# Kernel tuning notes

Measured on AMD Instinct MI355X. Metric: run time of the kernel, lower is better.

## Reference

```python
import jax, jax.numpy as jnp
import numpy as np

EPS = 1e-12  # matches F.normalize eps

def _l2norm(x):
    n = jnp.sqrt(jnp.sum(x * x, axis=-1, keepdims=True))
    return x / jnp.maximum(n, EPS)

def setup_inputs() -> dict:
    key = jax.random.key(0)
    k1, k2, k3, k4 = jax.random.split(key, 4)
    Bq, Lq, H = 32, 32, 768
    ppq = 8
    Bd, Ld = Bq * ppq, 512
    dim = 128
    q_hidden = jax.random.normal(k1, (Bq, Lq, H), dtype=jnp.float32)
    d_hidden = jax.random.normal(k2, (Bd, Ld, H), dtype=jnp.float32)
    W = jax.random.normal(k3, (dim, H), dtype=jnp.float32) * (1.0 / np.sqrt(H))
    d_mask = jax.random.randint(k4, (Bd, Ld), 0, 2).astype(bool)
    d_mask = d_mask.at[:, 0].set(True)  # guarantee >=1 valid token per doc
    return {"q_hidden": q_hidden, "d_hidden": d_hidden, "W": W,
            "d_mask": d_mask, "ppq": ppq}

def reference(q_hidden, d_hidden, W, d_mask, ppq):
    # linear projection (no bias) + L2 normalize, as in query()/doc()
    q = _l2norm(jnp.einsum('bqh,dh->bqd', q_hidden, W))        # [Bq, Lq, dim]
    d = _l2norm(jnp.einsum('bkh,dh->bkd', d_hidden, W))        # [Bd, Ld, dim]
    d = d * d_mask[..., None].astype(d.dtype)                  # zero masked tokens
    qd = jnp.repeat(q, ppq, axis=0)                            # [Bd, Lq, dim]
    sim = jnp.einsum('bqd,bkd->bqk', qd, d)                    # cosine MaxSim scores
    sim = jnp.where(d_mask[:, None, :], sim, -jnp.inf)         # mask doc tokens
    return jnp.sum(jnp.max(sim, axis=-1), axis=-1)             # [Bd]
```

## Files before the change

kernel.cpp:

```cpp
#include <hip/hip_runtime.h>
#include <math.h>

#define H    768
#define NT   24
#define DIM  128
#define LQ   32
#define LD   512
#define BM   128
#define EPSF 1e-12f

typedef _Float16 f16x8 __attribute__((ext_vector_type(8)));
typedef _Float16 f16x4 __attribute__((ext_vector_type(4)));
typedef float    f32x4 __attribute__((ext_vector_type(4)));

static __device__ __forceinline__ unsigned short h2u(_Float16 h) {
    return __builtin_bit_cast(unsigned short, h);
}

#define GLOAD_LDS16(g, l) __builtin_amdgcn_global_load_lds(                    \
    (const __attribute__((address_space(1))) unsigned int*)(const void*)(g),   \
    (__attribute__((address_space(3))) unsigned int*)(void*)(l), 16, 0, 0)

__global__ __launch_bounds__(256) void wconv_kernel(
    const float* __restrict__ W, unsigned short* __restrict__ wsW,
    float* __restrict__ WT)
{
    const int ks  = blockIdx.x;
    const int tid = threadIdx.x;
    #pragma unroll 4
    for (int i = 0; i < 16; ++i) {
        const int idx = tid + i * 256;
        const int row = idx >> 5, col = idx & 31;
        const float x = W[(size_t)row * H + ks * 32 + col];
        const int colS = (((col >> 3) ^ ((row >> 1) & 3)) << 3) | (col & 7);
        wsW[((size_t)ks * 128 + row) * 32 + colS] = h2u((_Float16)x);
        WT[((size_t)ks * 32 + col) * DIM + row] = x;
    }
}

__global__ __launch_bounds__(128) void qproj_kernel(
    const float* __restrict__ qh, const float* __restrict__ WT,
    unsigned short* __restrict__ qn)
{
    const int blk = blockIdx.x;
    const int tid = threadIdx.x;
    __shared__ float rows[4][H];
    __shared__ float red[128];

    const float4* src = (const float4*)(qh + (size_t)blk * 4 * H);
    float4*       dst = (float4*)&rows[0][0];
    for (int i = tid; i < 4 * H / 4; i += 128) dst[i] = src[i];
    __syncthreads();

    float acc[4] = {0.f, 0.f, 0.f, 0.f};
    #pragma unroll 8
    for (int h = 0; h < H; ++h) {
        const float wv = WT[(size_t)h * DIM + tid];
        acc[0] += wv * rows[0][h];
        acc[1] += wv * rows[1][h];
        acc[2] += wv * rows[2][h];
        acc[3] += wv * rows[3][h];
    }
    #pragma unroll
    for (int j = 0; j < 4; ++j) {
        red[tid] = acc[j] * acc[j];
        __syncthreads();
        for (int s = 64; s > 0; s >>= 1) {
            if (tid < s) red[tid] += red[tid + s];
            __syncthreads();
        }
        const float inv = 1.0f / fmaxf(sqrtf(red[0]), EPSF);
        qn[((size_t)blk * 4 + j) * DIM + tid] = h2u((_Float16)(acc[j] * inv));
        __syncthreads();
    }
}

struct Smem {
    union {
        struct {
            unsigned short A[2][BM][32];
            unsigned short Wt[2][128][32];
        } g;
        unsigned short C[BM][DIM];
    } u;
    float         pnorm[2][BM];
    unsigned char mk[BM];
    float         pmax[LQ][4];
};

__global__ __launch_bounds__(256, 4) void docgemm_kernel(
    const float* __restrict__ dh, const unsigned short* __restrict__ wsW,
    const int* __restrict__ dmask, const unsigned short* __restrict__ qn,
    float* __restrict__ part, const int* __restrict__ ppq_p)
{
    __shared__ Smem sm;
    const int blk = blockIdx.x;
    const int b   = blk >> 2;
    const int c   = blk & 3;
    const int tid = threadIdx.x;
    const int w   = tid >> 6;
    const int wm  = w >> 1, wn = w & 1;
    const int l   = tid & 63;
    const int g   = l >> 4;
    const int r15 = l & 15;
    const int ppq = ppq_p[0];

    const int r0   = tid >> 3;
    const int seg0 = tid & 7;
    const int aswz = (r0 >> 1) & 3;
    const int coli = (((seg0 >> 1) ^ aswz) << 3) | ((seg0 & 1) << 2);

    const float* Abase = dh + ((size_t)b * LD + (size_t)c * BM) * H;

    f32x4 acc[4][4];
    #pragma unroll
    for (int m = 0; m < 4; ++m)
        #pragma unroll
        for (int n = 0; n < 4; ++n)
            acc[m][n] = (f32x4){0.f, 0.f, 0.f, 0.f};

    float4 avA[4];

    {
        const char* wt   = (const char*)wsW;
        char*       wdst = (char*)&sm.u.g.Wt[0][0][0];
        GLOAD_LDS16(wt + tid * 16,        wdst + w * 1024);
        GLOAD_LDS16(wt + 4096 + tid * 16, wdst + 4096 + w * 1024);
        __builtin_amdgcn_sched_barrier(0);
        #pragma unroll
        for (int i = 0; i < 4; ++i)
            avA[i] = *(const float4*)(Abase + (size_t)(r0 + i * 32) * H + seg0 * 4);
        #pragma unroll
        for (int i = 0; i < 4; ++i) {
            const int row = r0 + i * 32;
            f16x4 h;
            h[0] = (_Float16)avA[i].x; h[1] = (_Float16)avA[i].y;
            h[2] = (_Float16)avA[i].z; h[3] = (_Float16)avA[i].w;
            *(f16x4*)&sm.u.g.A[0][row][coli] = h;
        }
        #pragma unroll
        for (int i = 0; i < 4; ++i)
            avA[i] = *(const float4*)(Abase + (size_t)(r0 + i * 32) * H + 32 + seg0 * 4);
        asm volatile("s_waitcnt vmcnt(4) lgkmcnt(0)" ::: "memory");
        __builtin_amdgcn_sched_barrier(0);
        __builtin_amdgcn_s_barrier();
        __builtin_amdgcn_sched_barrier(0);
    }

    for (int t = 0; t < NT; ++t) {
        const int cur = t & 1, nxt = cur ^ 1;

        if (t + 1 < NT) {
            const char* wt   = (const char*)wsW + (size_t)(t + 1) * 8192;
            char*       wdst = (char*)&sm.u.g.Wt[nxt][0][0];
            GLOAD_LDS16(wt + tid * 16,        wdst + w * 1024);
            GLOAD_LDS16(wt + 4096 + tid * 16, wdst + 4096 + w * 1024);
        }
        __builtin_amdgcn_sched_barrier(0);

        f16x8 ah[4];
        #pragma unroll
        for (int m = 0; m < 4; ++m) {
            const int row = wm * 64 + m * 16 + r15;
            const int sl  = (g ^ ((row >> 1) & 3)) * 8;
            ah[m] = *(const f16x8*)&sm.u.g.A[cur][row][sl];
        }
        __builtin_amdgcn_s_setprio(1);
        #pragma unroll
        for (int n = 0; n < 4; ++n) {
            const int row = wn * 64 + n * 16 + r15;
            const int sl  = (g ^ ((row >> 1) & 3)) * 8;
            f16x8 bh = *(const f16x8*)&sm.u.g.Wt[cur][row][sl];
            #pragma unroll
            for (int m = 0; m < 4; ++m)
                acc[m][n] = __builtin_amdgcn_mfma_f32_16x16x32_f16(ah[m], bh, acc[m][n], 0, 0, 0);
        }
        __builtin_amdgcn_s_setprio(0);

        if (t + 1 < NT) {
            #pragma unroll
            for (int i = 0; i < 4; ++i) {
                const int row = r0 + i * 32;
                f16x4 h;
                h[0] = (_Float16)avA[i].x; h[1] = (_Float16)avA[i].y;
                h[2] = (_Float16)avA[i].z; h[3] = (_Float16)avA[i].w;
                *(f16x4*)&sm.u.g.A[nxt][row][coli] = h;
            }
        }
        if (t + 2 < NT) {
            const int k0n = (t + 2) * 32;
            #pragma unroll
            for (int i = 0; i < 4; ++i)
                avA[i] = *(const float4*)(Abase + (size_t)(r0 + i * 32) * H + k0n + seg0 * 4);
        }

        if (t + 2 < NT) {
            asm volatile("s_waitcnt vmcnt(4) lgkmcnt(0)" ::: "memory");
        } else {
            asm volatile("s_waitcnt vmcnt(0) lgkmcnt(0)" ::: "memory");
        }
        __builtin_amdgcn_sched_barrier(0);
        __builtin_amdgcn_s_barrier();
        __builtin_amdgcn_sched_barrier(0);
    }

    #pragma unroll
    for (int m = 0; m < 4; ++m) {
        const int tokb = wm * 64 + m * 16 + g * 4;
        #pragma unroll
        for (int n = 0; n < 4; ++n) {
            const int dim = wn * 64 + n * 16 + r15;
            #pragma unroll
            for (int r = 0; r < 4; ++r) {
                const int tok  = tokb + r;
                const int slot = (dim >> 3) ^ (tok & 7);
                sm.u.C[tok][slot * 8 + (dim & 7)] = h2u((_Float16)acc[m][n][r]);
            }
        }
    }
    #pragma unroll
    for (int m = 0; m < 4; ++m) {
        #pragma unroll
        for (int r = 0; r < 4; ++r) {
            float s = 0.f;
            #pragma unroll
            for (int n = 0; n < 4; ++n) s += acc[m][n][r] * acc[m][n][r];
            s += __shfl_xor(s, 1); s += __shfl_xor(s, 2);
            s += __shfl_xor(s, 4); s += __shfl_xor(s, 8);
            if (r15 == 0) sm.pnorm[wn][wm * 64 + m * 16 + g * 4 + r] = s;
        }
    }
    if (tid < BM) sm.mk[tid] = (unsigned char)(dmask[(size_t)b * LD + c * BM + tid] != 0);
    __syncthreads();

    const unsigned short* qb = qn + (size_t)(b / ppq) * LQ * DIM;
    const int t0 = w * 32 + r15, t1 = t0 + 16;
    const float inv0 = 1.0f / fmaxf(sqrtf(sm.pnorm[0][t0] + sm.pnorm[1][t0]), EPSF);
    const float inv1 = 1.0f / fmaxf(sqrtf(sm.pnorm[0][t1] + sm.pnorm[1][t1]), EPSF);

    f32x4 sacc[2][2];
    #pragma unroll
    for (int m = 0; m < 2; ++m)
        #pragma unroll
        for (int n = 0; n < 2; ++n)
            sacc[m][n] = (f32x4){0.f, 0.f, 0.f, 0.f};
    #pragma unroll
    for (int ks = 0; ks < 4; ++ks) {
        f16x8 qa[2], cb[2];
        #pragma unroll
        for (int m = 0; m < 2; ++m)
            qa[m] = *(const f16x8*)(qb + (size_t)(m * 16 + r15) * DIM + ks * 32 + g * 8);
        #pragma unroll
        for (int n = 0; n < 2; ++n) {
            const int row  = w * 32 + n * 16 + r15;
            const int slot = (ks * 4 + g) ^ (row & 7);
            cb[n] = *(const f16x8*)&sm.u.C[row][slot * 8];
        }
        #pragma unroll
        for (int m = 0; m < 2; ++m)
            #pragma unroll
            for (int n = 0; n < 2; ++n)
                sacc[m][n] = __builtin_amdgcn_mfma_f32_16x16x32_f16(qa[m], cb[n], sacc[m][n], 0, 0, 0);
    }

    const int m0 = sm.mk[t0], m1 = sm.mk[t1];
    #pragma unroll
    for (int m = 0; m < 2; ++m) {
        #pragma unroll
        for (int r = 0; r < 4; ++r) {
            float v0 = m0 ? sacc[m][0][r] * inv0 : -INFINITY;
            float v1 = m1 ? sacc[m][1][r] * inv1 : -INFINITY;
            float vmax = fmaxf(v0, v1);
            vmax = fmaxf(vmax, __shfl_xor(vmax, 1));
            vmax = fmaxf(vmax, __shfl_xor(vmax, 2));
            vmax = fmaxf(vmax, __shfl_xor(vmax, 4));
            vmax = fmaxf(vmax, __shfl_xor(vmax, 8));
            if (r15 == 0) sm.pmax[m * 16 + g * 4 + r][w] = vmax;
        }
    }
    __syncthreads();
    if (tid < LQ) {
        float mv = fmaxf(fmaxf(sm.pmax[tid][0], sm.pmax[tid][1]),
                         fmaxf(sm.pmax[tid][2], sm.pmax[tid][3]));
        part[(size_t)blk * 32 + tid] = mv;
    }
}

__global__ __launch_bounds__(64) void final_kernel(
    const float* __restrict__ part, float* __restrict__ out)
{
    const int b = blockIdx.x;
    const int q = threadIdx.x & 31;
    const float* p = part + (size_t)b * 128;
    float m = fmaxf(fmaxf(p[q], p[32 + q]), fmaxf(p[64 + q], p[96 + q]));
    #pragma unroll
    for (int off = 1; off < 32; off <<= 1) m += __shfl_xor(m, off);
    if (threadIdx.x == 0) out[b] = m;
}

extern "C" void kernel_launch(void* const* d_in, const int* in_sizes, int n_in,
                              void* d_out, int out_size, void* d_ws, size_t ws_size,
                              hipStream_t stream) {
    const float* qh    = (const float*)d_in[0];
    const float* dh    = (const float*)d_in[1];
    const float* W     = (const float*)d_in[2];
    const int*   dmask = (const int*)d_in[3];
    const int*   ppq   = (const int*)d_in[4];
    float*       out   = (float*)d_out;

    unsigned short* wsW  = (unsigned short*)d_ws;
    float*          WT   = (float*)((char*)d_ws + 196608);
    unsigned short* qn   = (unsigned short*)((char*)d_ws + 589824);
    float*          part = (float*)((char*)d_ws + 851968);

    const int nq = in_sizes[0] / H;
    const int Bd = out_size;

    wconv_kernel<<<NT, 256, 0, stream>>>(W, wsW, WT);
    qproj_kernel<<<nq / 4, 128, 0, stream>>>(qh, WT, qn);
    docgemm_kernel<<<Bd * 4, 256, 0, stream>>>(dh, wsW, dmask, qn, part, ppq);
    final_kernel<<<Bd, 64, 0, stream>>>(part, out);
}
```

Baseline: 131.5 us.

## Double K-tile to 64, use 8-wave doc GEMM blocks, split qproj reduction

The doc projection GEMM now uses a K step of 64 instead of 32, so there are 12 pipeline iterations instead of 24. It runs 512-thread blocks arranged as a 2x4 wave grid, with a matching XOR swizzle for the wider LDS rows. The MaxSim epilogue is remapped so each of the 8 waves handles 16 tokens, and the query projection splits the H reduction across two thread halves. The aim is fewer barriers per byte streamed and more memory-level parallelism on the bandwidth-bound fp32 doc read. The cost is double the LDS per block, which limits residency to 2 blocks per CU and may reduce latency hiding.

```diff
diff --git a/kernel.cpp b/kernel.cpp
--- a/kernel.cpp
+++ b/kernel.cpp
@@ -2,7 +2,7 @@
 #include <math.h>
 
 #define H    768
-#define NT   24
+#define NT   12
 #define DIM  128
 #define LQ   32
 #define LD   512
@@ -27,50 +27,59 @@
 {
     const int ks  = blockIdx.x;
     const int tid = threadIdx.x;
-    #pragma unroll 4
-    for (int i = 0; i < 16; ++i) {
+    #pragma unroll 8
+    for (int i = 0; i < 32; ++i) {
         const int idx = tid + i * 256;
-        const int row = idx >> 5, col = idx & 31;
-        const float x = W[(size_t)row * H + ks * 32 + col];
-        const int colS = (((col >> 3) ^ ((row >> 1) & 3)) << 3) | (col & 7);
-        wsW[((size_t)ks * 128 + row) * 32 + colS] = h2u((_Float16)x);
-        WT[((size_t)ks * 32 + col) * DIM + row] = x;
-    }
-}
-
-__global__ __launch_bounds__(128) void qproj_kernel(
+        const int row = idx >> 6, col = idx & 63;
+        const float x = W[(size_t)row * H + ks * 64 + col];
+        const int colS = (((col >> 3) ^ (row & 7)) << 3) | (col & 7);
+        wsW[((size_t)ks * 128 + row) * 64 + colS] = h2u((_Float16)x);
+        WT[((size_t)ks * 64 + col) * DIM + row] = x;
+    }
+}
+
+__global__ __launch_bounds__(256) void qproj_kernel(
     const float* __restrict__ qh, const float* __restrict__ WT,
     unsigned short* __restrict__ qn)
 {
     const int blk = blockIdx.x;
     const int tid = threadIdx.x;
+    const int td  = tid & 127;
+    const int hp  = tid >> 7;
     __shared__ float rows[4][H];
+    __shared__ float psum[2][4][128];
     __shared__ float red[128];
 
     const float4* src = (const float4*)(qh + (size_t)blk * 4 * H);
     float4*       dst = (float4*)&rows[0][0];
-    for (int i = tid; i < 4 * H / 4; i += 128) dst[i] = src[i];
+    for (int i = tid; i < 4 * H / 4; i += 256) dst[i] = src[i];
     __syncthreads();
 
     float acc[4] = {0.f, 0.f, 0.f, 0.f};
+    const int h0 = hp * (H / 2);
     #pragma unroll 8
-    for (int h = 0; h < H; ++h) {
-        const float wv = WT[(size_t)h * DIM + tid];
+    for (int h = h0; h < h0 + H / 2; ++h) {
+        const float wv = WT[(size_t)h * DIM + td];
         acc[0] += wv * rows[0][h];
         acc[1] += wv * rows[1][h];
         acc[2] += wv * rows[2][h];
         acc[3] += wv * rows[3][h];
     }
     #pragma unroll
+    for (int j = 0; j < 4; ++j) psum[hp][j][td] = acc[j];
+    __syncthreads();
+
+    #pragma unroll
     for (int j = 0; j < 4; ++j) {
-        red[tid] = acc[j] * acc[j];
+        const float val = psum[0][j][td] + psum[1][j][td];
+        if (hp == 0) red[td] = val * val;
         __syncthreads();
         for (int s = 64; s > 0; s >>= 1) {
             if (tid < s) red[tid] += red[tid + s];
             __syncthreads();
         }
         const float inv = 1.0f / fmaxf(sqrtf(red[0]), EPSF);
-        qn[((size_t)blk * 4 + j) * DIM + tid] = h2u((_Float16)(acc[j] * inv));
+        if (hp == 0) qn[((size_t)blk * 4 + j) * DIM + td] = h2u((_Float16)(val * inv));
         __syncthreads();
     }
 }
@@ -78,17 +87,17 @@
 struct Smem {
     union {
         struct {
-            unsigned short A[2][BM][32];
-            unsigned short Wt[2][128][32];
+            unsigned short A[2][BM][64];
+            unsigned short Wt[2][128][64];
         } g;
         unsigned short C[BM][DIM];
     } u;
-    float         pnorm[2][BM];
+    float         pnorm[4][BM];
     unsigned char mk[BM];
-    float         pmax[LQ][4];
+    float         pmax[LQ][8];
 };
 
-__global__ __launch_bounds__(256, 4) void docgemm_kernel(
+__global__ __launch_bounds__(512, 2) void docgemm_kernel(
     const float* __restrict__ dh, const unsigned short* __restrict__ wsW,
     const int* __restrict__ dmask, const unsigned short* __restrict__ qn,
     float* __restrict__ part, const int* __restrict__ ppq_p)
@@ -99,24 +108,25 @@
     const int c   = blk & 3;
     const int tid = threadIdx.x;
     const int w   = tid >> 6;
-    const int wm  = w >> 1, wn = w & 1;
+    const int wm  = w >> 2;
+    const int wn  = w & 3;
     const int l   = tid & 63;
     const int g   = l >> 4;
     const int r15 = l & 15;
     const int ppq = ppq_p[0];
 
-    const int r0   = tid >> 3;
-    const int seg0 = tid & 7;
-    const int aswz = (r0 >> 1) & 3;
-    const int coli = (((seg0 >> 1) ^ aswz) << 3) | ((seg0 & 1) << 2);
+    const int r0   = tid >> 4;
+    const int seg0 = tid & 15;
+    const int wgr  = seg0 >> 1;
+    const int wsub = (seg0 & 1) * 8;
 
     const float* Abase = dh + ((size_t)b * LD + (size_t)c * BM) * H;
 
-    f32x4 acc[4][4];
+    f32x4 acc[4][2];
     #pragma unroll
     for (int m = 0; m < 4; ++m)
         #pragma unroll
-        for (int n = 0; n < 4; ++n)
+        for (int n = 0; n < 2; ++n)
             acc[m][n] = (f32x4){0.f, 0.f, 0.f, 0.f};
 
     float4 avA[4];
@@ -125,7 +135,7 @@
         const char* wt   = (const char*)wsW;
         char*       wdst = (char*)&sm.u.g.Wt[0][0][0];
         GLOAD_LDS16(wt + tid * 16,        wdst + w * 1024);
-        GLOAD_LDS16(wt + 4096 + tid * 16, wdst + 4096 + w * 1024);
+        GLOAD_LDS16(wt + 8192 + tid * 16, wdst + 8192 + w * 1024);
         __builtin_amdgcn_sched_barrier(0);
         #pragma unroll
         for (int i = 0; i < 4; ++i)
@@ -136,11 +146,11 @@
             f16x4 h;
             h[0] = (_Float16)avA[i].x; h[1] = (_Float16)avA[i].y;
             h[2] = (_Float16)avA[i].z; h[3] = (_Float16)avA[i].w;
-            *(f16x4*)&sm.u.g.A[0][row][coli] = h;
+            *(f16x4*)((char*)&sm.u.g.A[0][0][0] + row * 128 + (((wgr ^ (row & 7)) << 4) | wsub)) = h;
         }
         #pragma unroll
         for (int i = 0; i < 4; ++i)
-            avA[i] = *(const float4*)(Abase + (size_t)(r0 + i * 32) * H + 32 + seg0 * 4);
+            avA[i] = *(const float4*)(Abase + (size_t)(r0 + i * 32) * H + 64 + seg0 * 4);
         asm volatile("s_waitcnt vmcnt(4) lgkmcnt(0)" ::: "memory");
         __builtin_amdgcn_sched_barrier(0);
         __builtin_amdgcn_s_barrier();
@@ -151,29 +161,34 @@
         const int cur = t & 1, nxt = cur ^ 1;
 
         if (t + 1 < NT) {
-            const char* wt   = (const char*)wsW + (size_t)(t + 1) * 8192;
+            const char* wt   = (const char*)wsW + (size_t)(t + 1) * 16384;
             char*       wdst = (char*)&sm.u.g.Wt[nxt][0][0];
             GLOAD_LDS16(wt + tid * 16,        wdst + w * 1024);
-            GLOAD_LDS16(wt + 4096 + tid * 16, wdst + 4096 + w * 1024);
-        }
-        __builtin_amdgcn_sched_barrier(0);
-
-        f16x8 ah[4];
-        #pragma unroll
-        for (int m = 0; m < 4; ++m) {
-            const int row = wm * 64 + m * 16 + r15;
-            const int sl  = (g ^ ((row >> 1) & 3)) * 8;
-            ah[m] = *(const f16x8*)&sm.u.g.A[cur][row][sl];
-        }
+            GLOAD_LDS16(wt + 8192 + tid * 16, wdst + 8192 + w * 1024);
+        }
+        __builtin_amdgcn_sched_barrier(0);
+
+        const char* Ab = (const char*)&sm.u.g.A[cur][0][0];
+        const char* Wb = (const char*)&sm.u.g.Wt[cur][0][0];
+        f16x8 ah[2][4];
+        #pragma unroll
+        for (int ksub = 0; ksub < 2; ++ksub)
+            #pragma unroll
+            for (int m = 0; m < 4; ++m) {
+                const int row = wm * 64 + m * 16 + r15;
+                ah[ksub][m] = *(const f16x8*)(Ab + row * 128 + ((((ksub * 4 + g)) ^ (row & 7)) << 4));
+            }
         __builtin_amdgcn_s_setprio(1);
         #pragma unroll
-        for (int n = 0; n < 4; ++n) {
-            const int row = wn * 64 + n * 16 + r15;
-            const int sl  = (g ^ ((row >> 1) & 3)) * 8;
-            f16x8 bh = *(const f16x8*)&sm.u.g.Wt[cur][row][sl];
-            #pragma unroll
-            for (int m = 0; m < 4; ++m)
-                acc[m][n] = __builtin_amdgcn_mfma_f32_16x16x32_f16(ah[m], bh, acc[m][n], 0, 0, 0);
+        for (int ksub = 0; ksub < 2; ++ksub) {
+            #pragma unroll
+            for (int n = 0; n < 2; ++n) {
+                const int row = wn * 32 + n * 16 + r15;
+                f16x8 bh = *(const f16x8*)(Wb + row * 128 + ((((ksub * 4 + g)) ^ (row & 7)) << 4));
+                #pragma unroll
+                for (int m = 0; m < 4; ++m)
+                    acc[m][n] = __builtin_amdgcn_mfma_f32_16x16x32_f16(ah[ksub][m], bh, acc[m][n], 0, 0, 0);
+            }
         }
         __builtin_amdgcn_s_setprio(0);
 
@@ -184,11 +199,11 @@
                 f16x4 h;
                 h[0] = (_Float16)avA[i].x; h[1] = (_Float16)avA[i].y;
                 h[2] = (_Float16)avA[i].z; h[3] = (_Float16)avA[i].w;
-                *(f16x4*)&sm.u.g.A[nxt][row][coli] = h;
+                *(f16x4*)((char*)&sm.u.g.A[nxt][0][0] + row * 128 + (((wgr ^ (row & 7)) << 4) | wsub)) = h;
             }
         }
         if (t + 2 < NT) {
-            const int k0n = (t + 2) * 32;
+            const int k0n = (t + 2) * 64;
             #pragma unroll
             for (int i = 0; i < 4; ++i)
                 avA[i] = *(const float4*)(Abase + (size_t)(r0 + i * 32) * H + k0n + seg0 * 4);
@@ -208,8 +223,8 @@
     for (int m = 0; m < 4; ++m) {
         const int tokb = wm * 64 + m * 16 + g * 4;
         #pragma unroll
-        for (int n = 0; n < 4; ++n) {
-            const int dim = wn * 64 + n * 16 + r15;
+        for (int n = 0; n < 2; ++n) {
+            const int dim = wn * 32 + n * 16 + r15;
             #pragma unroll
             for (int r = 0; r < 4; ++r) {
                 const int tok  = tokb + r;
@@ -222,9 +237,7 @@
     for (int m = 0; m < 4; ++m) {
         #pragma unroll
         for (int r = 0; r < 4; ++r) {
-            float s = 0.f;
-            #pragma unroll
-            for (int n = 0; n < 4; ++n) s += acc[m][n][r] * acc[m][n][r];
+            float s = acc[m][0][r] * acc[m][0][r] + acc[m][1][r] * acc[m][1][r];
             s += __shfl_xor(s, 1); s += __shfl_xor(s, 2);
             s += __shfl_xor(s, 4); s += __shfl_xor(s, 8);
             if (r15 == 0) sm.pnorm[wn][wm * 64 + m * 16 + g * 4 + r] = s;
@@ -234,54 +247,42 @@
     __syncthreads();
 
     const unsigned short* qb = qn + (size_t)(b / ppq) * LQ * DIM;
-    const int t0 = w * 32 + r15, t1 = t0 + 16;
-    const float inv0 = 1.0f / fmaxf(sqrtf(sm.pnorm[0][t0] + sm.pnorm[1][t0]), EPSF);
-    const float inv1 = 1.0f / fmaxf(sqrtf(sm.pnorm[0][t1] + sm.pnorm[1][t1]), EPSF);
-
-    f32x4 sacc[2][2];
-    #pragma unroll
-    for (int m = 0; m < 2; ++m)
-        #pragma unroll
-        for (int n = 0; n < 2; ++n)
-            sacc[m][n] = (f32x4){0.f, 0.f, 0.f, 0.f};
+    const int tok = w * 16 + r15;
+    const float inv = 1.0f / fmaxf(sqrtf(sm.pnorm[0][tok] + sm.pnorm[1][tok] +
+                                         sm.pnorm[2][tok] + sm.pnorm[3][tok]), EPSF);
+    const int msk = sm.mk[tok];
+
+    f32x4 sacc[2];
+    sacc[0] = (f32x4){0.f, 0.f, 0.f, 0.f};
+    sacc[1] = (f32x4){0.f, 0.f, 0.f, 0.f};
     #pragma unroll
     for (int ks = 0; ks < 4; ++ks) {
-        f16x8 qa[2], cb[2];
-        #pragma unroll
-        for (int m = 0; m < 2; ++m)
-            qa[m] = *(const f16x8*)(qb + (size_t)(m * 16 + r15) * DIM + ks * 32 + g * 8);
-        #pragma unroll
-        for (int n = 0; n < 2; ++n) {
-            const int row  = w * 32 + n * 16 + r15;
-            const int slot = (ks * 4 + g) ^ (row & 7);
-            cb[n] = *(const f16x8*)&sm.u.C[row][slot * 8];
-        }
-        #pragma unroll
-        for (int m = 0; m < 2; ++m)
-            #pragma unroll
-            for (int n = 0; n < 2; ++n)
-                sacc[m][n] = __builtin_amdgcn_mfma_f32_16x16x32_f16(qa[m], cb[n], sacc[m][n], 0, 0, 0);
-    }
-
-    const int m0 = sm.mk[t0], m1 = sm.mk[t1];
+        const int slot = (ks * 4 + g) ^ (tok & 7);
+        f16x8 cb = *(const f16x8*)&sm.u.C[tok][slot * 8];
+        #pragma unroll
+        for (int m = 0; m < 2; ++m) {
+            f16x8 qa = *(const f16x8*)(qb + (size_t)(m * 16 + r15) * DIM + ks * 32 + g * 8);
+            sacc[m] = __builtin_amdgcn_mfma_f32_16x16x32_f16(qa, cb, sacc[m], 0, 0, 0);
+        }
+    }
+
     #pragma unroll
     for (int m = 0; m < 2; ++m) {
         #pragma unroll
         for (int r = 0; r < 4; ++r) {
-            float v0 = m0 ? sacc[m][0][r] * inv0 : -INFINITY;
-            float v1 = m1 ? sacc[m][1][r] * inv1 : -INFINITY;
-            float vmax = fmaxf(v0, v1);
-            vmax = fmaxf(vmax, __shfl_xor(vmax, 1));
-            vmax = fmaxf(vmax, __shfl_xor(vmax, 2));
-            vmax = fmaxf(vmax, __shfl_xor(vmax, 4));
-            vmax = fmaxf(vmax, __shfl_xor(vmax, 8));
-            if (r15 == 0) sm.pmax[m * 16 + g * 4 + r][w] = vmax;
+            float v = msk ? sacc[m][r] * inv : -INFINITY;
+            v = fmaxf(v, __shfl_xor(v, 1));
+            v = fmaxf(v, __shfl_xor(v, 2));
+            v = fmaxf(v, __shfl_xor(v, 4));
+            v = fmaxf(v, __shfl_xor(v, 8));
+            if (r15 == 0) sm.pmax[m * 16 + g * 4 + r][w] = v;
         }
     }
     __syncthreads();
     if (tid < LQ) {
-        float mv = fmaxf(fmaxf(sm.pmax[tid][0], sm.pmax[tid][1]),
-                         fmaxf(sm.pmax[tid][2], sm.pmax[tid][3]));
+        float mv = sm.pmax[tid][0];
+        #pragma unroll
+        for (int j = 1; j < 8; ++j) mv = fmaxf(mv, sm.pmax[tid][j]);
         part[(size_t)blk * 32 + tid] = mv;
     }
 }
@@ -317,7 +318,7 @@
     const int Bd = out_size;
 
     wconv_kernel<<<NT, 256, 0, stream>>>(W, wsW, WT);
-    qproj_kernel<<<nq / 4, 128, 0, stream>>>(qh, WT, qn);
-    docgemm_kernel<<<Bd * 4, 256, 0, stream>>>(dh, wsW, dmask, qn, part, ppq);
+    qproj_kernel<<<nq / 4, 256, 0, stream>>>(qh, WT, qn);
+    docgemm_kernel<<<Bd * 4, 512, 0, stream>>>(dh, wsW, dmask, qn, part, ppq);
     final_kernel<<<Bd, 64, 0, stream>>>(part, out);
 }
```

Result: slower. 194.1 us (+47.6%).

## Deepen doc GEMM A-tile register prefetch and split query projection over hidden dimension

Applied to the files above, without the earlier changes.

The doc GEMM main loop is unrolled by two and uses two register buffers for the fp32 A tiles. Global loads now run three K-steps ahead and are issued before the MFMA block, so more HBM latency is hidden on this bandwidth-bound stream. The query projection kernel doubles its threads and splits the 768-wide reduction into two halves combined through shared memory, to shorten its serial dot-product loop. The extra live float4 registers raise VGPR pressure under launch_bounds(256,4), which could cost occupancy or cause spills.

```diff
diff --git a/kernel.cpp b/kernel.cpp
--- a/kernel.cpp
+++ b/kernel.cpp
@@ -38,39 +38,48 @@
     }
 }
 
-__global__ __launch_bounds__(128) void qproj_kernel(
+__global__ __launch_bounds__(256) void qproj_kernel(
     const float* __restrict__ qh, const float* __restrict__ WT,
     unsigned short* __restrict__ qn)
 {
     const int blk = blockIdx.x;
     const int tid = threadIdx.x;
+    const int td  = tid & 127;
+    const int hp  = tid >> 7;
     __shared__ float rows[4][H];
+    __shared__ float psum[2][4][128];
     __shared__ float red[128];
 
     const float4* src = (const float4*)(qh + (size_t)blk * 4 * H);
     float4*       dst = (float4*)&rows[0][0];
-    for (int i = tid; i < 4 * H / 4; i += 128) dst[i] = src[i];
+    for (int i = tid; i < 4 * H / 4; i += 256) dst[i] = src[i];
     __syncthreads();
 
     float acc[4] = {0.f, 0.f, 0.f, 0.f};
+    const int h0 = hp * (H / 2);
     #pragma unroll 8
-    for (int h = 0; h < H; ++h) {
-        const float wv = WT[(size_t)h * DIM + tid];
+    for (int h = h0; h < h0 + H / 2; ++h) {
+        const float wv = WT[(size_t)h * DIM + td];
         acc[0] += wv * rows[0][h];
         acc[1] += wv * rows[1][h];
         acc[2] += wv * rows[2][h];
         acc[3] += wv * rows[3][h];
     }
     #pragma unroll
+    for (int j = 0; j < 4; ++j) psum[hp][j][td] = acc[j];
+    __syncthreads();
+
+    #pragma unroll
     for (int j = 0; j < 4; ++j) {
-        red[tid] = acc[j] * acc[j];
+        const float val = psum[0][j][td] + psum[1][j][td];
+        if (hp == 0) red[td] = val * val;
         __syncthreads();
         for (int s = 64; s > 0; s >>= 1) {
             if (tid < s) red[tid] += red[tid + s];
             __syncthreads();
         }
         const float inv = 1.0f / fmaxf(sqrtf(red[0]), EPSF);
-        qn[((size_t)blk * 4 + j) * DIM + tid] = h2u((_Float16)(acc[j] * inv));
+        if (hp == 0) qn[((size_t)blk * 4 + j) * DIM + td] = h2u((_Float16)(val * inv));
         __syncthreads();
     }
 }
@@ -87,6 +96,62 @@
     unsigned char mk[BM];
     float         pmax[LQ][4];
 };
+
+#define KSTEP(T, CUR, NXT, AV)                                                  \
+  {                                                                             \
+    if ((T) + 1 < NT) {                                                         \
+      const char* wt_   = (const char*)wsW + (size_t)((T) + 1) * 8192;          \
+      char*       wdst_ = (char*)&sm.u.g.Wt[NXT][0][0];                         \
+      GLOAD_LDS16(wt_ + tid * 16,        wdst_ + w * 1024);                     \
+      GLOAD_LDS16(wt_ + 4096 + tid * 16, wdst_ + 4096 + w * 1024);              \
+    }                                                                           \
+    __builtin_amdgcn_sched_barrier(0);                                          \
+    if ((T) + 1 < NT) {                                                         \
+      _Pragma("unroll")                                                         \
+      for (int i = 0; i < 4; ++i) {                                             \
+        const int row_ = r0 + i * 32;                                           \
+        f16x4 h_;                                                               \
+        h_[0] = (_Float16)AV[i].x; h_[1] = (_Float16)AV[i].y;                   \
+        h_[2] = (_Float16)AV[i].z; h_[3] = (_Float16)AV[i].w;                   \
+        *(f16x4*)&sm.u.g.A[NXT][row_][coli] = h_;                               \
+      }                                                                         \
+    }                                                                           \
+    if ((T) + 3 < NT) {                                                         \
+      const int k0n_ = ((T) + 3) * 32;                                          \
+      _Pragma("unroll")                                                         \
+      for (int i = 0; i < 4; ++i)                                               \
+        AV[i] = *(const float4*)(Abase + (size_t)(r0 + i * 32) * H + k0n_ + seg0 * 4); \
+    }                                                                           \
+    __builtin_amdgcn_sched_barrier(0);                                          \
+    {                                                                           \
+      f16x8 ah_[4];                                                             \
+      _Pragma("unroll")                                                         \
+      for (int m = 0; m < 4; ++m) {                                             \
+        const int row_ = wm * 64 + m * 16 + r15;                                \
+        const int sl_  = (g ^ ((row_ >> 1) & 3)) * 8;                           \
+        ah_[m] = *(const f16x8*)&sm.u.g.A[CUR][row_][sl_];                      \
+      }                                                                         \
+      __builtin_amdgcn_s_setprio(1);                                            \
+      _Pragma("unroll")                                                         \
+      for (int n = 0; n < 4; ++n) {                                             \
+        const int row_ = wn * 64 + n * 16 + r15;                                \
+        const int sl_  = (g ^ ((row_ >> 1) & 3)) * 8;                           \
+        f16x8 bh_ = *(const f16x8*)&sm.u.g.Wt[CUR][row_][sl_];                  \
+        _Pragma("unroll")                                                       \
+        for (int m = 0; m < 4; ++m)                                             \
+          acc[m][n] = __builtin_amdgcn_mfma_f32_16x16x32_f16(ah_[m], bh_, acc[m][n], 0, 0, 0); \
+      }                                                                         \
+      __builtin_amdgcn_s_setprio(0);                                            \
+    }                                                                           \
+    if ((T) + 3 < NT) {                                                         \
+      asm volatile("s_waitcnt vmcnt(4) lgkmcnt(0)" ::: "memory");               \
+    } else {                                                                    \
+      asm volatile("s_waitcnt vmcnt(0) lgkmcnt(0)" ::: "memory");               \
+    }                                                                           \
+    __builtin_amdgcn_sched_barrier(0);                                          \
+    __builtin_amdgcn_s_barrier();                                               \
+    __builtin_amdgcn_sched_barrier(0);                                          \
+  }
 
 __global__ __launch_bounds__(256, 4) void docgemm_kernel(
     const float* __restrict__ dh, const unsigned short* __restrict__ wsW,
@@ -119,7 +184,7 @@
         for (int n = 0; n < 4; ++n)
             acc[m][n] = (f32x4){0.f, 0.f, 0.f, 0.f};
 
-    float4 avA[4];
+    float4 avA0[4], avA1[4];
 
     {
         const char* wt   = (const char*)wsW;
@@ -129,79 +194,30 @@
         __builtin_amdgcn_sched_barrier(0);
         #pragma unroll
         for (int i = 0; i < 4; ++i)
-            avA[i] = *(const float4*)(Abase + (size_t)(r0 + i * 32) * H + seg0 * 4);
+            avA0[i] = *(const float4*)(Abase + (size_t)(r0 + i * 32) * H + seg0 * 4);
+        #pragma unroll
+        for (int i = 0; i < 4; ++i)
+            avA1[i] = *(const float4*)(Abase + (size_t)(r0 + i * 32) * H + 32 + seg0 * 4);
         #pragma unroll
         for (int i = 0; i < 4; ++i) {
             const int row = r0 + i * 32;
             f16x4 h;
-            h[0] = (_Float16)avA[i].x; h[1] = (_Float16)avA[i].y;
-            h[2] = (_Float16)avA[i].z; h[3] = (_Float16)avA[i].w;
+            h[0] = (_Float16)avA0[i].x; h[1] = (_Float16)avA0[i].y;
+            h[2] = (_Float16)avA0[i].z; h[3] = (_Float16)avA0[i].w;
             *(f16x4*)&sm.u.g.A[0][row][coli] = h;
         }
         #pragma unroll
         for (int i = 0; i < 4; ++i)
-            avA[i] = *(const float4*)(Abase + (size_t)(r0 + i * 32) * H + 32 + seg0 * 4);
-        asm volatile("s_waitcnt vmcnt(4) lgkmcnt(0)" ::: "memory");
+            avA0[i] = *(const float4*)(Abase + (size_t)(r0 + i * 32) * H + 64 + seg0 * 4);
+        asm volatile("s_waitcnt lgkmcnt(0)" ::: "memory");
         __builtin_amdgcn_sched_barrier(0);
         __builtin_amdgcn_s_barrier();
         __builtin_amdgcn_sched_barrier(0);
     }
 
-    for (int t = 0; t < NT; ++t) {
-        const int cur = t & 1, nxt = cur ^ 1;
-
-        if (t + 1 < NT) {
-            const char* wt   = (const char*)wsW + (size_t)(t + 1) * 8192;
-            char*       wdst = (char*)&sm.u.g.Wt[nxt][0][0];
-            GLOAD_LDS16(wt + tid * 16,        wdst + w * 1024);
-            GLOAD_LDS16(wt + 4096 + tid * 16, wdst + 4096 + w * 1024);
-        }
-        __builtin_amdgcn_sched_barrier(0);
-
-        f16x8 ah[4];
-        #pragma unroll
-        for (int m = 0; m < 4; ++m) {
-            const int row = wm * 64 + m * 16 + r15;
-            const int sl  = (g ^ ((row >> 1) & 3)) * 8;
-            ah[m] = *(const f16x8*)&sm.u.g.A[cur][row][sl];
-        }
-        __builtin_amdgcn_s_setprio(1);
-        #pragma unroll
-        for (int n = 0; n < 4; ++n) {
-            const int row = wn * 64 + n * 16 + r15;
-            const int sl  = (g ^ ((row >> 1) & 3)) * 8;
-            f16x8 bh = *(const f16x8*)&sm.u.g.Wt[cur][row][sl];
-            #pragma unroll
-            for (int m = 0; m < 4; ++m)
-                acc[m][n] = __builtin_amdgcn_mfma_f32_16x16x32_f16(ah[m], bh, acc[m][n], 0, 0, 0);
-        }
-        __builtin_amdgcn_s_setprio(0);
-
-        if (t + 1 < NT) {
-            #pragma unroll
-            for (int i = 0; i < 4; ++i) {
-                const int row = r0 + i * 32;
-                f16x4 h;
-                h[0] = (_Float16)avA[i].x; h[1] = (_Float16)avA[i].y;
-                h[2] = (_Float16)avA[i].z; h[3] = (_Float16)avA[i].w;
-                *(f16x4*)&sm.u.g.A[nxt][row][coli] = h;
-            }
-        }
-        if (t + 2 < NT) {
-            const int k0n = (t + 2) * 32;
-            #pragma unroll
-            for (int i = 0; i < 4; ++i)
-                avA[i] = *(const float4*)(Abase + (size_t)(r0 + i * 32) * H + k0n + seg0 * 4);
-        }
-
-        if (t + 2 < NT) {
-            asm volatile("s_waitcnt vmcnt(4) lgkmcnt(0)" ::: "memory");
-        } else {
-            asm volatile("s_waitcnt vmcnt(0) lgkmcnt(0)" ::: "memory");
-        }
-        __builtin_amdgcn_sched_barrier(0);
-        __builtin_amdgcn_s_barrier();
-        __builtin_amdgcn_sched_barrier(0);
+    for (int tt = 0; tt < NT; tt += 2) {
+        KSTEP(tt,     0, 1, avA1)
+        KSTEP(tt + 1, 1, 0, avA0)
     }
 
     #pragma unroll
@@ -317,7 +333,7 @@
     const int Bd = out_size;
 
     wconv_kernel<<<NT, 256, 0, stream>>>(W, wsW, WT);
-    qproj_kernel<<<nq / 4, 128, 0, stream>>>(qh, WT, qn);
+    qproj_kernel<<<nq / 4, 256, 0, stream>>>(qh, WT, qn);
     docgemm_kernel<<<Bd * 4, 256, 0, stream>>>(dh, wsW, dmask, qn, part, ppq);
     final_kernel<<<Bd, 64, 0, stream>>>(part, out);
 }
```

Result: slower. 215.6 us (+63.9%).

## Compact valid doc tokens and skip fully-masked tiles in doc GEMM

Applied to the files above, without the earlier changes.

Adds a compaction kernel that builds per-document lists of unmasked token indices and counts. The doc GEMM gathers only valid rows through these indices and exits early for 128-row tiles lying beyond the valid count, so the projection of masked tokens is never computed or loaded. With roughly half the tokens masked, this should remove about half of the d_hidden traffic and MFMA work. The query projection is also split across two half-warps over H, doubling its threads. The cost is an extra kernel launch and gathered, less contiguous row loads.

```diff
diff --git a/kernel.cpp b/kernel.cpp
--- a/kernel.cpp
+++ b/kernel.cpp
@@ -20,6 +20,23 @@
 #define GLOAD_LDS16(g, l) __builtin_amdgcn_global_load_lds(                    \
     (const __attribute__((address_space(1))) unsigned int*)(const void*)(g),   \
     (__attribute__((address_space(3))) unsigned int*)(void*)(l), 16, 0, 0)
+
+__global__ __launch_bounds__(64) void compact_kernel(
+    const int* __restrict__ dmask, int* __restrict__ idx, int* __restrict__ cnt)
+{
+    const int b = blockIdx.x;
+    const int l = threadIdx.x;
+    int base = 0;
+    for (int t0 = 0; t0 < LD; t0 += 64) {
+        const int v = dmask[(size_t)b * LD + t0 + l] != 0;
+        const unsigned long long bal = __ballot(v);
+        const int pre = __popcll(bal & ((1ULL << l) - 1ULL));
+        if (v) idx[(size_t)b * LD + base + pre] = t0 + l;
+        base += (int)__popcll(bal);
+    }
+    for (int j = base + l; j < LD; j += 64) idx[(size_t)b * LD + j] = 0;
+    if (l == 0) cnt[b] = base;
+}
 
 __global__ __launch_bounds__(256) void wconv_kernel(
     const float* __restrict__ W, unsigned short* __restrict__ wsW,
@@ -38,39 +55,48 @@
     }
 }
 
-__global__ __launch_bounds__(128) void qproj_kernel(
+__global__ __launch_bounds__(256) void qproj_kernel(
     const float* __restrict__ qh, const float* __restrict__ WT,
     unsigned short* __restrict__ qn)
 {
     const int blk = blockIdx.x;
     const int tid = threadIdx.x;
+    const int td  = tid & 127;
+    const int hp  = tid >> 7;
     __shared__ float rows[4][H];
+    __shared__ float psum[2][4][128];
     __shared__ float red[128];
 
     const float4* src = (const float4*)(qh + (size_t)blk * 4 * H);
     float4*       dst = (float4*)&rows[0][0];
-    for (int i = tid; i < 4 * H / 4; i += 128) dst[i] = src[i];
+    for (int i = tid; i < 4 * H / 4; i += 256) dst[i] = src[i];
     __syncthreads();
 
     float acc[4] = {0.f, 0.f, 0.f, 0.f};
+    const int h0 = hp * (H / 2);
     #pragma unroll 8
-    for (int h = 0; h < H; ++h) {
-        const float wv = WT[(size_t)h * DIM + tid];
+    for (int h = h0; h < h0 + H / 2; ++h) {
+        const float wv = WT[(size_t)h * DIM + td];
         acc[0] += wv * rows[0][h];
         acc[1] += wv * rows[1][h];
         acc[2] += wv * rows[2][h];
         acc[3] += wv * rows[3][h];
     }
     #pragma unroll
+    for (int j = 0; j < 4; ++j) psum[hp][j][td] = acc[j];
+    __syncthreads();
+
+    #pragma unroll
     for (int j = 0; j < 4; ++j) {
-        red[tid] = acc[j] * acc[j];
+        const float val = psum[0][j][td] + psum[1][j][td];
+        if (hp == 0) red[td] = val * val;
         __syncthreads();
         for (int s = 64; s > 0; s >>= 1) {
             if (tid < s) red[tid] += red[tid + s];
             __syncthreads();
         }
         const float inv = 1.0f / fmaxf(sqrtf(red[0]), EPSF);
-        qn[((size_t)blk * 4 + j) * DIM + tid] = h2u((_Float16)(acc[j] * inv));
+        if (hp == 0) qn[((size_t)blk * 4 + j) * DIM + td] = h2u((_Float16)(val * inv));
         __syncthreads();
     }
 }
@@ -84,20 +110,27 @@
         unsigned short C[BM][DIM];
     } u;
     float         pnorm[2][BM];
-    unsigned char mk[BM];
     float         pmax[LQ][4];
 };
 
 __global__ __launch_bounds__(256, 4) void docgemm_kernel(
     const float* __restrict__ dh, const unsigned short* __restrict__ wsW,
-    const int* __restrict__ dmask, const unsigned short* __restrict__ qn,
+    const int* __restrict__ idxl, const int* __restrict__ cnt,
+    const unsigned short* __restrict__ qn,
     float* __restrict__ part, const int* __restrict__ ppq_p)
 {
-    __shared__ Smem sm;
     const int blk = blockIdx.x;
     const int b   = blk >> 2;
     const int c   = blk & 3;
     const int tid = threadIdx.x;
+    const int cntb = cnt[b];
+
+    if (c * BM >= cntb) {
+        if (tid < LQ) part[(size_t)blk * 32 + tid] = -INFINITY;
+        return;
+    }
+
+    __shared__ Smem sm;
     const int w   = tid >> 6;
     const int wm  = w >> 1, wn = w & 1;
     const int l   = tid & 63;
@@ -110,7 +143,11 @@
     const int aswz = (r0 >> 1) & 3;
     const int coli = (((seg0 >> 1) ^ aswz) << 3) | ((seg0 & 1) << 2);
 
-    const float* Abase = dh + ((size_t)b * LD + (size_t)c * BM) * H;
+    const int* idxb = idxl + (size_t)b * LD + c * BM;
+    const float* Ar0 = dh + ((size_t)b * LD + idxb[r0])      * H + seg0 * 4;
+    const float* Ar1 = dh + ((size_t)b * LD + idxb[r0 + 32]) * H + seg0 * 4;
+    const float* Ar2 = dh + ((size_t)b * LD + idxb[r0 + 64]) * H + seg0 * 4;
+    const float* Ar3 = dh + ((size_t)b * LD + idxb[r0 + 96]) * H + seg0 * 4;
 
     f32x4 acc[4][4];
     #pragma unroll
@@ -127,9 +164,10 @@
         GLOAD_LDS16(wt + tid * 16,        wdst + w * 1024);
         GLOAD_LDS16(wt + 4096 + tid * 16, wdst + 4096 + w * 1024);
         __builtin_amdgcn_sched_barrier(0);
-        #pragma unroll
-        for (int i = 0; i < 4; ++i)
-            avA[i] = *(const float4*)(Abase + (size_t)(r0 + i * 32) * H + seg0 * 4);
+        avA[0] = *(const float4*)(Ar0);
+        avA[1] = *(const float4*)(Ar1);
+        avA[2] = *(const float4*)(Ar2);
+        avA[3] = *(const float4*)(Ar3);
         #pragma unroll
         for (int i = 0; i < 4; ++i) {
             const int row = r0 + i * 32;
@@ -138,9 +176,10 @@
             h[2] = (_Float16)avA[i].z; h[3] = (_Float16)avA[i].w;
             *(f16x4*)&sm.u.g.A[0][row][coli] = h;
         }
-        #pragma unroll
-        for (int i = 0; i < 4; ++i)
-            avA[i] = *(const float4*)(Abase + (size_t)(r0 + i * 32) * H + 32 + seg0 * 4);
+        avA[0] = *(const float4*)(Ar0 + 32);
+        avA[1] = *(const float4*)(Ar1 + 32);
+        avA[2] = *(const float4*)(Ar2 + 32);
+        avA[3] = *(const float4*)(Ar3 + 32);
         asm volatile("s_waitcnt vmcnt(4) lgkmcnt(0)" ::: "memory");
         __builtin_amdgcn_sched_barrier(0);
         __builtin_amdgcn_s_barrier();
@@ -189,9 +228,10 @@
         }
         if (t + 2 < NT) {
             const int k0n = (t + 2) * 32;
-            #pragma unroll
-            for (int i = 0; i < 4; ++i)
-                avA[i] = *(const float4*)(Abase + (size_t)(r0 + i * 32) * H + k0n + seg0 * 4);
+            avA[0] = *(const float4*)(Ar0 + k0n);
+            avA[1] = *(const float4*)(Ar1 + k0n);
+            avA[2] = *(const float4*)(Ar2 + k0n);
+            avA[3] = *(const float4*)(Ar3 + k0n);
         }
 
         if (t + 2 < NT) {
@@ -230,7 +270,6 @@
             if (r15 == 0) sm.pnorm[wn][wm * 64 + m * 16 + g * 4 + r] = s;
         }
     }
-    if (tid < BM) sm.mk[tid] = (unsigned char)(dmask[(size_t)b * LD + c * BM + tid] != 0);
     __syncthreads();
 
     const unsigned short* qb = qn + (size_t)(b / ppq) * LQ * DIM;
@@ -263,7 +302,8 @@
                 sacc[m][n] = __builtin_amdgcn_mfma_f32_16x16x32_f16(qa[m], cb[n], sacc[m][n], 0, 0, 0);
     }
 
-    const int m0 = sm.mk[t0], m1 = sm.mk[t1];
+    const int m0 = (c * BM + t0) < cntb;
+    const int m1 = (c * BM + t1) < cntb;
     #pragma unroll
     for (int m = 0; m < 2; ++m) {
         #pragma unroll
@@ -312,12 +352,15 @@
     float*          WT   = (float*)((char*)d_ws + 196608);
     unsigned short* qn   = (unsigned short*)((char*)d_ws + 589824);
     float*          part = (float*)((char*)d_ws + 851968);
+    int*            idx  = (int*)((char*)d_ws + 983040);
+    int*            cnt  = (int*)((char*)d_ws + 1507328);
 
     const int nq = in_sizes[0] / H;
     const int Bd = out_size;
 
+    compact_kernel<<<Bd, 64, 0, stream>>>(dmask, idx, cnt);
     wconv_kernel<<<NT, 256, 0, stream>>>(W, wsW, WT);
-    qproj_kernel<<<nq / 4, 128, 0, stream>>>(qh, WT, qn);
-    docgemm_kernel<<<Bd * 4, 256, 0, stream>>>(dh, wsW, dmask, qn, part, ppq);
+    qproj_kernel<<<nq / 4, 256, 0, stream>>>(qh, WT, qn);
+    docgemm_kernel<<<Bd * 4, 256, 0, stream>>>(dh, wsW, idx, cnt, qn, part, ppq);
     final_kernel<<<Bd, 64, 0, stream>>>(part, out);
 }
```

Result: slower. 184.6 us (+40.3%).
